# Performance work log

Measured on AMD Instinct MI355X. Metric: run time of the kernel, lower is better.

Reference implementation:

```python
import jax, jax.numpy as jnp
import numpy as np

N_NODES = 20000
N_EDGES = 640000
IN_DIM, HIDDEN, OUT_DIM = 128, 256, 64
EPS = 1e-12


def setup_inputs() -> dict:
    key = jax.random.key(0)
    ks = jax.random.split(key, 8)
    x = jax.random.normal(ks[0], (N_NODES, IN_DIM), dtype=jnp.float32)
    edge_src = jax.random.randint(ks[1], (N_EDGES,), 0, N_NODES, dtype=jnp.int32)
    edge_dst = jax.random.randint(ks[2], (N_EDGES,), 0, N_NODES, dtype=jnp.int32)
    s1 = 1.0 / np.sqrt(IN_DIM)
    s2 = 1.0 / np.sqrt(HIDDEN)
    W1 = jax.random.uniform(ks[3], (IN_DIM, HIDDEN), jnp.float32, -s1, s1)
    b1 = jax.random.uniform(ks[4], (HIDDEN,), jnp.float32, -s1, s1)
    W2 = jax.random.uniform(ks[5], (HIDDEN, OUT_DIM), jnp.float32, -s2, s2)
    b2 = jax.random.uniform(ks[6], (OUT_DIM,), jnp.float32, -s2, s2)
    return {"x": x, "edge_src": edge_src, "edge_dst": edge_dst,
            "W1": W1, "b1": b1, "W2": W2, "b2": b2}


def _agnn_layer(h, src, dst, n_nodes):
    # AGNN propagation with beta = 1 (non-trainable buffer in source module):
    # out_i = sum_j softmax_j(cos(h_i, h_j)) * h_j over neighbors j (incl. self-loop)
    hn = h * jax.lax.rsqrt(jnp.sum(h * h, axis=-1, keepdims=True) + EPS)
    logits = jnp.sum(hn[src] * hn[dst], axis=-1)            # [E] cosine similarity
    m = jax.ops.segment_max(logits, dst, num_segments=n_nodes)
    e = jnp.exp(logits - m[dst])
    z = jax.ops.segment_sum(e, dst, num_segments=n_nodes)
    alpha = e / z[dst]                                       # per-dst softmax
    return jax.ops.segment_sum(alpha[:, None] * h[src], dst, num_segments=n_nodes)


def reference(x, edge_src, edge_dst, W1, b1, W2, b2):
    n = x.shape[0]
    loop = jnp.arange(n, dtype=edge_src.dtype)
    src = jnp.concatenate([edge_src, loop])
    dst = jnp.concatenate([edge_dst, loop])
    h = jax.nn.relu(x @ W1 + b1)
    for _ in range(4):
        h = jax.nn.relu(_agnn_layer(h, src, dst, n))
    return h @ W2 + b2
```

## Files before the change

### kernel.cpp

```cpp
#include <hip/hip_runtime.h>

#define N_NODES 20000
#define N_EDGES 640000
#define E_TOT   (N_EDGES + N_NODES)
#define IN_DIM  128
#define HIDDEN  256
#define OUT_DIM 64
#define LOG2E 1.4426950408889634f

typedef __attribute__((ext_vector_type(8))) short short8;

__device__ __forceinline__ float bf2f(unsigned short u) {
    union { unsigned int i; float f; } x; x.i = ((unsigned int)u) << 16; return x.f;
}
__device__ __forceinline__ unsigned short f2bf(float f) {
    union { float f; unsigned int i; } x; x.f = f;
    unsigned int u = x.i;
    return (unsigned short)((u + 0x7fffu + ((u >> 16) & 1u)) >> 16);
}


__global__ void zero_cnt_kernel(int* __restrict__ cnt) {
    int i = blockIdx.x * blockDim.x + threadIdx.x;
    if (i < N_NODES) cnt[i] = 0;
}

__global__ void count_kernel(const int* __restrict__ edge_dst, int* __restrict__ cnt) {
    int i = blockIdx.x * blockDim.x + threadIdx.x;
    if (i >= E_TOT) return;
    int d = (i < N_EDGES) ? edge_dst[i] : (i - N_EDGES);
    atomicAdd(&cnt[d], 1);
}

__global__ __launch_bounds__(1024) void scan_kernel(int* __restrict__ cnt, int* __restrict__ indptr) {
    const int T = 1024;
    const int C = (N_NODES + T - 1) / T;
    __shared__ int sums[T];
    int t = threadIdx.x;
    int base = t * C;
    int local[C];
    int s = 0;
#pragma unroll
    for (int i = 0; i < C; i++) {
        int idx = base + i;
        int v = (idx < N_NODES) ? cnt[idx] : 0;
        local[i] = s;
        s += v;
    }
    sums[t] = s;
    __syncthreads();
    for (int off = 1; off < T; off <<= 1) {
        int v = (t >= off) ? sums[t - off] : 0;
        __syncthreads();
        sums[t] += v;
        __syncthreads();
    }
    int prefix = (t == 0) ? 0 : sums[t - 1];
#pragma unroll
    for (int i = 0; i < C; i++) {
        int idx = base + i;
        if (idx < N_NODES) {
            indptr[idx] = prefix + local[i];
            cnt[idx] = 0;
        }
    }
    if (t == T - 1) indptr[N_NODES] = prefix + s;
}

__global__ void scatter_kernel(const int* __restrict__ edge_src, const int* __restrict__ edge_dst,
                               const int* __restrict__ indptr, int* __restrict__ cnt,
                               int* __restrict__ ssrc) {
    int i = blockIdx.x * blockDim.x + threadIdx.x;
    if (i >= E_TOT) return;
    int d, s;
    if (i < N_EDGES) { d = edge_dst[i]; s = edge_src[i]; }
    else             { d = i - N_EDGES; s = d; }
    int pos = indptr[d] + atomicAdd(&cnt[d], 1);
    ssrc[pos] = s;
}


__global__ __launch_bounds__(256) void gemm_bias_act(const float* __restrict__ A,
                                                     const float* __restrict__ B,
                                                     const float* __restrict__ bias,
                                                     float* __restrict__ C,
                                                     int M, int Nn, int K, int relu) {
    __shared__ float As[16][65];
    __shared__ float Bs[16][65];
    int tid = threadIdx.x;
    int tx = tid & 15, ty = tid >> 4;
    int row0 = blockIdx.x * 64, col0 = blockIdx.y * 64;
    float acc[4][4] = {};
    for (int k0 = 0; k0 < K; k0 += 16) {
        {
            int r_ = tid >> 2;
            int kq = (tid & 3) * 4;
            int gr = row0 + r_;
            float4 a4 = make_float4(0.f, 0.f, 0.f, 0.f);
            if (gr < M) a4 = *(const float4*)&A[(long)gr * K + k0 + kq];
            As[kq + 0][r_] = a4.x; As[kq + 1][r_] = a4.y;
            As[kq + 2][r_] = a4.z; As[kq + 3][r_] = a4.w;
        }
        {
            int kr = tid >> 4;
            int cq = (tid & 15) * 4;
            float4 b4 = *(const float4*)&B[(long)(k0 + kr) * Nn + col0 + cq];
            Bs[kr][cq + 0] = b4.x; Bs[kr][cq + 1] = b4.y;
            Bs[kr][cq + 2] = b4.z; Bs[kr][cq + 3] = b4.w;
        }
        __syncthreads();
#pragma unroll
        for (int kk = 0; kk < 16; kk++) {
            float a[4], b[4];
#pragma unroll
            for (int i = 0; i < 4; i++) a[i] = As[kk][ty * 4 + i];
#pragma unroll
            for (int j = 0; j < 4; j++) b[j] = Bs[kk][tx * 4 + j];
#pragma unroll
            for (int i = 0; i < 4; i++)
#pragma unroll
                for (int j = 0; j < 4; j++) acc[i][j] += a[i] * b[j];
        }
        __syncthreads();
    }
#pragma unroll
    for (int i = 0; i < 4; i++) {
        int gr = row0 + ty * 4 + i;
        if (gr >= M) continue;
#pragma unroll
        for (int j = 0; j < 4; j++) {
            int gc = col0 + tx * 4 + j;
            float v = acc[i][j] + bias[gc];
            if (relu) v = fmaxf(v, 0.f);
            C[(long)gr * Nn + gc] = v;
        }
    }
}


__global__ __launch_bounds__(256) void normalize0_kernel(const float* __restrict__ h,
                                                         unsigned short* __restrict__ hnb,
                                                         float* __restrict__ r) {
    int i = blockIdx.x;
    int c = threadIdx.x;
    float v = h[(long)i * HIDDEN + c];
    float ss = v * v;
#pragma unroll
    for (int off = 32; off; off >>= 1) ss += __shfl_xor(ss, off);
    __shared__ float wsum[4];
    int wid = c >> 6, lane = c & 63;
    if (lane == 0) wsum[wid] = ss;
    __syncthreads();
    float tot = wsum[0] + wsum[1] + wsum[2] + wsum[3];
    float rr = sqrtf(tot + 1e-12f);
    hnb[(long)i * HIDDEN + c] = f2bf(v / rr);
    if (c == 0) r[i] = rr;
}


__global__ __launch_bounds__(256) void agnn_kernel(const unsigned short* __restrict__ hnb,
                                                   const float* __restrict__ rin,
                                                   const int* __restrict__ indptr,
                                                   const int* __restrict__ ssrc,
                                                   unsigned short* __restrict__ hnout,
                                                   float* __restrict__ rout,
                                                   float* __restrict__ hout,
                                                   int write_hn) {
    int wid = threadIdx.x >> 6;
    int lane = threadIdx.x & 63;
    int node = blockIdx.x * 4 + wid;
    if (node >= N_NODES) return;
    int l32 = lane & 31;
    int halfid = lane >> 5;

    const short8* tab = (const short8*)hnb;
    short8 hdv = tab[(long)node * 32 + l32];
    float hd[8];
#pragma unroll
    for (int j = 0; j < 8; j++) hd[j] = bf2f((unsigned short)hdv[j]);

    int beg = indptr[node], end = indptr[node + 1];
    int deg = end - beg;
    int cA = (deg + 1) >> 1;
    int cnt = halfid ? (deg - cA) : cA;
    int eb = beg + (halfid ? cA : 0);

    float m2 = -INFINITY, z = 0.f;
    float acc[8] = {0.f, 0.f, 0.f, 0.f, 0.f, 0.f, 0.f, 0.f};

    int s0 = (cnt > 0) ? ssrc[eb] : 0;
    short8 v = tab[(long)s0 * 32 + l32];
    float rs = rin[s0];

    for (int i = 0; i < cnt; i++) {
        short8 cv = v;
        float crs = rs;
        if (i + 1 < cnt) {
            int sn = ssrc[eb + i + 1];
            v = tab[(long)sn * 32 + l32];
            rs = rin[sn];
        }
        float cf[8];
        float dot = 0.f;
#pragma unroll
        for (int j = 0; j < 8; j++) { cf[j] = bf2f((unsigned short)cv[j]); dot += hd[j] * cf[j]; }
#pragma unroll
        for (int off = 16; off; off >>= 1) dot += __shfl_xor(dot, off);
        float d2 = dot * LOG2E;
        if (d2 <= m2) {
            float w = exp2f(d2 - m2);
            z += w;
            float wr = w * crs;
#pragma unroll
            for (int j = 0; j < 8; j++) acc[j] += wr * cf[j];
        } else {
            float sc = exp2f(m2 - d2);
            z = z * sc + 1.f;
#pragma unroll
            for (int j = 0; j < 8; j++) acc[j] = acc[j] * sc + crs * cf[j];
            m2 = d2;
        }
    }

    float om = __shfl_xor(m2, 32);
    float oz = __shfl_xor(z, 32);
    float oa[8];
#pragma unroll
    for (int j = 0; j < 8; j++) oa[j] = __shfl_xor(acc[j], 32);
    float nm = fmaxf(m2, om);
    float sA = exp2f(m2 - nm);
    float sB = exp2f(om - nm);
    z = z * sA + oz * sB;
    float inv = 1.f / z;
    float o[8];
#pragma unroll
    for (int j = 0; j < 8; j++) o[j] = fmaxf((acc[j] * sA + oa[j] * sB) * inv, 0.f);

    if (write_hn) {
        float ss = 0.f;
#pragma unroll
        for (int j = 0; j < 8; j++) ss += o[j] * o[j];
#pragma unroll
        for (int off = 16; off; off >>= 1) ss += __shfl_xor(ss, off);
        float rr = sqrtf(ss + 1e-12f);
        if (halfid == 0) {
            float irr = 1.f / rr;
            short8 ov;
#pragma unroll
            for (int j = 0; j < 8; j++) ov[j] = (short)f2bf(o[j] * irr);
            ((short8*)hnout)[(long)node * 32 + l32] = ov;
            if (l32 == 0) rout[node] = rr;
        }
    } else {
        if (halfid == 0) {
            float4 lo = make_float4(o[0], o[1], o[2], o[3]);
            float4 hi = make_float4(o[4], o[5], o[6], o[7]);
            ((float4*)hout)[(long)node * 64 + l32 * 2] = lo;
            ((float4*)hout)[(long)node * 64 + l32 * 2 + 1] = hi;
        }
    }
}


extern "C" void kernel_launch(void* const* d_in, const int* in_sizes, int n_in,
                              void* d_out, int out_size, void* d_ws, size_t ws_size,
                              hipStream_t stream) {
    const float* x  = (const float*)d_in[0];
    const int* esrc = (const int*)d_in[1];
    const int* edst = (const int*)d_in[2];
    const float* W1 = (const float*)d_in[3];
    const float* b1 = (const float*)d_in[4];
    const float* W2 = (const float*)d_in[5];
    const float* b2 = (const float*)d_in[6];
    float* out = (float*)d_out;

    char* ws = (char*)d_ws;
    float*          h0     = (float*)(ws);
    unsigned short* hnA    = (unsigned short*)(ws + 20480000);
    unsigned short* hnB    = (unsigned short*)(ws + 30720000);
    float*          rA     = (float*)(ws + 40960000);
    float*          rB     = (float*)(ws + 41040000);
    int*            indptr = (int*)  (ws + 41120000);
    int*            cnt    = (int*)  (ws + 41200256);
    int*            ssrc   = (int*)  (ws + 41280256);

    zero_cnt_kernel<<<(N_NODES + 255) / 256, 256, 0, stream>>>(cnt);
    count_kernel<<<(E_TOT + 255) / 256, 256, 0, stream>>>(edst, cnt);
    scan_kernel<<<1, 1024, 0, stream>>>(cnt, indptr);
    scatter_kernel<<<(E_TOT + 255) / 256, 256, 0, stream>>>(esrc, edst, indptr, cnt, ssrc);

    dim3 g1((N_NODES + 63) / 64, HIDDEN / 64);
    gemm_bias_act<<<g1, 256, 0, stream>>>(x, W1, b1, h0, N_NODES, HIDDEN, IN_DIM, 1);

    normalize0_kernel<<<N_NODES, 256, 0, stream>>>(h0, hnA, rA);

    int nblk = (N_NODES + 3) / 4;
    agnn_kernel<<<nblk, 256, 0, stream>>>(hnA, rA, indptr, ssrc, hnB, rB, h0, 1);
    agnn_kernel<<<nblk, 256, 0, stream>>>(hnB, rB, indptr, ssrc, hnA, rA, h0, 1);
    agnn_kernel<<<nblk, 256, 0, stream>>>(hnA, rA, indptr, ssrc, hnB, rB, h0, 1);
    agnn_kernel<<<nblk, 256, 0, stream>>>(hnB, rB, indptr, ssrc, hnA, rA, h0, 0);

    dim3 g2((N_NODES + 63) / 64, OUT_DIM / 64);
    gemm_bias_act<<<g2, 256, 0, stream>>>(h0, W2, b2, out, N_NODES, OUT_DIM, HIDDEN, 0);
}
```

Baseline: 364.8 us.

## Map 16 lanes per node in AGNN and drop online max rescaling

Each wavefront now handles four nodes with 16 lanes apiece, each lane holding 16 bf16 features loaded as two uint4, where before one node was split across two 32-lane halves. The online-softmax max tracking is removed because cosine logits are bounded by one, so exp2 is applied directly and the cross-half merge disappears. It also uses packed float2 arithmetic, pre-scales the destination vector by log2e, and turns the prefetch into a clamped branchless load. The aim is fewer idle lanes, more parallel nodes, and less control flow and shuffle work. In exchange the bounds check is gone, since the node count divides evenly by 16, and the skipped max subtraction depends on the logits staying bounded.

Result: faster. 349.2 us (-4.3%).

```diff
diff --git a/kernel.cpp b/kernel.cpp
--- a/kernel.cpp
+++ b/kernel.cpp
@@ -8,15 +8,21 @@
 #define OUT_DIM 64
 #define LOG2E 1.4426950408889634f
 
-typedef __attribute__((ext_vector_type(8))) short short8;
-
-__device__ __forceinline__ float bf2f(unsigned short u) {
-    union { unsigned int i; float f; } x; x.i = ((unsigned int)u) << 16; return x.f;
-}
+typedef __attribute__((ext_vector_type(2))) float f32x2;
+
 __device__ __forceinline__ unsigned short f2bf(float f) {
     union { float f; unsigned int i; } x; x.f = f;
     unsigned int u = x.i;
     return (unsigned short)((u + 0x7fffu + ((u >> 16) & 1u)) >> 16);
+}
+__device__ __forceinline__ f32x2 up2(unsigned int p) {
+    f32x2 r;
+    r.x = __uint_as_float(p << 16);
+    r.y = __uint_as_float(p & 0xffff0000u);
+    return r;
+}
+__device__ __forceinline__ unsigned int pk2(float a, float b) {
+    return (unsigned int)f2bf(a) | ((unsigned int)f2bf(b) << 16);
 }
 
 
@@ -166,98 +172,113 @@
                                                    float* __restrict__ rout,
                                                    float* __restrict__ hout,
                                                    int write_hn) {
-    int wid = threadIdx.x >> 6;
     int lane = threadIdx.x & 63;
-    int node = blockIdx.x * 4 + wid;
-    if (node >= N_NODES) return;
-    int l32 = lane & 31;
-    int halfid = lane >> 5;
-
-    const short8* tab = (const short8*)hnb;
-    short8 hdv = tab[(long)node * 32 + l32];
-    float hd[8];
-#pragma unroll
-    for (int j = 0; j < 8; j++) hd[j] = bf2f((unsigned short)hdv[j]);
+    int wid  = threadIdx.x >> 6;
+    int gid  = lane >> 4;
+    int gl   = lane & 15;
+    int node = blockIdx.x * 16 + wid * 4 + gid;
+
+    const uint4* tab4 = (const uint4*)hnb;
+    long nb = (long)node * 32 + gl * 2;
+    uint4 ha = tab4[nb], hb = tab4[nb + 1];
+    f32x2 hd2[8];
+    {
+        f32x2 t;
+        t = up2(ha.x); hd2[0] = t * LOG2E;
+        t = up2(ha.y); hd2[1] = t * LOG2E;
+        t = up2(ha.z); hd2[2] = t * LOG2E;
+        t = up2(ha.w); hd2[3] = t * LOG2E;
+        t = up2(hb.x); hd2[4] = t * LOG2E;
+        t = up2(hb.y); hd2[5] = t * LOG2E;
+        t = up2(hb.z); hd2[6] = t * LOG2E;
+        t = up2(hb.w); hd2[7] = t * LOG2E;
+    }
 
     int beg = indptr[node], end = indptr[node + 1];
-    int deg = end - beg;
-    int cA = (deg + 1) >> 1;
-    int cnt = halfid ? (deg - cA) : cA;
-    int eb = beg + (halfid ? cA : 0);
-
-    float m2 = -INFINITY, z = 0.f;
-    float acc[8] = {0.f, 0.f, 0.f, 0.f, 0.f, 0.f, 0.f, 0.f};
-
-    int s0 = (cnt > 0) ? ssrc[eb] : 0;
-    short8 v = tab[(long)s0 * 32 + l32];
-    float rs = rin[s0];
-
-    for (int i = 0; i < cnt; i++) {
-        short8 cv = v;
-        float crs = rs;
-        if (i + 1 < cnt) {
-            int sn = ssrc[eb + i + 1];
-            v = tab[(long)sn * 32 + l32];
-            rs = rin[sn];
-        }
-        float cf[8];
-        float dot = 0.f;
-#pragma unroll
-        for (int j = 0; j < 8; j++) { cf[j] = bf2f((unsigned short)cv[j]); dot += hd[j] * cf[j]; }
-#pragma unroll
-        for (int off = 16; off; off >>= 1) dot += __shfl_xor(dot, off);
-        float d2 = dot * LOG2E;
-        if (d2 <= m2) {
-            float w = exp2f(d2 - m2);
-            z += w;
-            float wr = w * crs;
-#pragma unroll
-            for (int j = 0; j < 8; j++) acc[j] += wr * cf[j];
-        } else {
-            float sc = exp2f(m2 - d2);
-            z = z * sc + 1.f;
-#pragma unroll
-            for (int j = 0; j < 8; j++) acc[j] = acc[j] * sc + crs * cf[j];
-            m2 = d2;
-        }
-    }
-
-    float om = __shfl_xor(m2, 32);
-    float oz = __shfl_xor(z, 32);
-    float oa[8];
-#pragma unroll
-    for (int j = 0; j < 8; j++) oa[j] = __shfl_xor(acc[j], 32);
-    float nm = fmaxf(m2, om);
-    float sA = exp2f(m2 - nm);
-    float sB = exp2f(om - nm);
-    z = z * sA + oz * sB;
+    int n = end - beg;
+    int last = end - 1;
+
+    f32x2 acc[8];
+#pragma unroll
+    for (int p = 0; p < 8; p++) acc[p] = (f32x2)0.f;
+    float z = 0.f;
+
+    int s = ssrc[beg];
+    long sb = (long)s * 32 + gl * 2;
+    uint4 va = tab4[sb], vb = tab4[sb + 1];
+    float rs = rin[s];
+
+    for (int i = 0; i < n; i++) {
+        uint4 ca = va, cb = vb;
+        float cr = rs;
+        {
+            int nx = beg + i + 1;
+            nx = (nx > last) ? last : nx;
+            int s2 = ssrc[nx];
+            long b2 = (long)s2 * 32 + gl * 2;
+            va = tab4[b2]; vb = tab4[b2 + 1];
+            rs = rin[s2];
+        }
+        f32x2 cf[8];
+        cf[0] = up2(ca.x); cf[1] = up2(ca.y); cf[2] = up2(ca.z); cf[3] = up2(ca.w);
+        cf[4] = up2(cb.x); cf[5] = up2(cb.y); cf[6] = up2(cb.z); cf[7] = up2(cb.w);
+        f32x2 d2a = cf[0] * hd2[0];
+        f32x2 d2b = cf[1] * hd2[1];
+        d2a += cf[2] * hd2[2];  d2b += cf[3] * hd2[3];
+        d2a += cf[4] * hd2[4];  d2b += cf[5] * hd2[5];
+        d2a += cf[6] * hd2[6];  d2b += cf[7] * hd2[7];
+        f32x2 d2 = d2a + d2b;
+        float d = d2.x + d2.y;
+        d += __shfl_xor(d, 1, 16);
+        d += __shfl_xor(d, 2, 16);
+        d += __shfl_xor(d, 4, 16);
+        d += __shfl_xor(d, 8, 16);
+        float w = exp2f(d);
+        z += w;
+        float wr = w * cr;
+#pragma unroll
+        for (int p = 0; p < 8; p++) acc[p] += cf[p] * wr;
+    }
+
     float inv = 1.f / z;
-    float o[8];
-#pragma unroll
-    for (int j = 0; j < 8; j++) o[j] = fmaxf((acc[j] * sA + oa[j] * sB) * inv, 0.f);
+    f32x2 o[8];
+#pragma unroll
+    for (int p = 0; p < 8; p++) {
+        f32x2 t = acc[p] * inv;
+        t.x = fmaxf(t.x, 0.f);
+        t.y = fmaxf(t.y, 0.f);
+        o[p] = t;
+    }
 
     if (write_hn) {
         float ss = 0.f;
 #pragma unroll
-        for (int j = 0; j < 8; j++) ss += o[j] * o[j];
-#pragma unroll
-        for (int off = 16; off; off >>= 1) ss += __shfl_xor(ss, off);
+        for (int p = 0; p < 8; p++) ss += o[p].x * o[p].x + o[p].y * o[p].y;
+        ss += __shfl_xor(ss, 1, 16);
+        ss += __shfl_xor(ss, 2, 16);
+        ss += __shfl_xor(ss, 4, 16);
+        ss += __shfl_xor(ss, 8, 16);
         float rr = sqrtf(ss + 1e-12f);
-        if (halfid == 0) {
-            float irr = 1.f / rr;
-            short8 ov;
-#pragma unroll
-            for (int j = 0; j < 8; j++) ov[j] = (short)f2bf(o[j] * irr);
-            ((short8*)hnout)[(long)node * 32 + l32] = ov;
-            if (l32 == 0) rout[node] = rr;
-        }
+        float ir = 1.f / rr;
+        uint4 oa, ob;
+        oa.x = pk2(o[0].x * ir, o[0].y * ir);
+        oa.y = pk2(o[1].x * ir, o[1].y * ir);
+        oa.z = pk2(o[2].x * ir, o[2].y * ir);
+        oa.w = pk2(o[3].x * ir, o[3].y * ir);
+        ob.x = pk2(o[4].x * ir, o[4].y * ir);
+        ob.y = pk2(o[5].x * ir, o[5].y * ir);
+        ob.z = pk2(o[6].x * ir, o[6].y * ir);
+        ob.w = pk2(o[7].x * ir, o[7].y * ir);
+        uint4* outt = (uint4*)hnout;
+        outt[nb] = oa;
+        outt[nb + 1] = ob;
+        if (gl == 0) rout[node] = rr;
     } else {
-        if (halfid == 0) {
-            float4 lo = make_float4(o[0], o[1], o[2], o[3]);
-            float4 hi = make_float4(o[4], o[5], o[6], o[7]);
-            ((float4*)hout)[(long)node * 64 + l32 * 2] = lo;
-            ((float4*)hout)[(long)node * 64 + l32 * 2 + 1] = hi;
-        }
+        float4* ho = (float4*)(hout + (long)node * HIDDEN + gl * 16);
+        ho[0] = make_float4(o[0].x, o[0].y, o[1].x, o[1].y);
+        ho[1] = make_float4(o[2].x, o[2].y, o[3].x, o[3].y);
+        ho[2] = make_float4(o[4].x, o[4].y, o[5].x, o[5].y);
+        ho[3] = make_float4(o[6].x, o[6].y, o[7].x, o[7].y);
     }
 }
 
@@ -294,7 +315,7 @@
 
     normalize0_kernel<<<N_NODES, 256, 0, stream>>>(h0, hnA, rA);
 
-    int nblk = (N_NODES + 3) / 4;
+    int nblk = N_NODES / 16;
     agnn_kernel<<<nblk, 256, 0, stream>>>(hnA, rA, indptr, ssrc, hnB, rB, h0, 1);
     agnn_kernel<<<nblk, 256, 0, stream>>>(hnB, rB, indptr, ssrc, hnA, rA, h0, 1);
     agnn_kernel<<<nblk, 256, 0, stream>>>(hnA, rA, indptr, ssrc, hnB, rB, h0, 1);
```
